# Kernel tuning notes

Measured on AMD Instinct MI355X. Metric: run time of the kernel, lower is better.

The kernel has to match this reference:

```python
import jax, jax.numpy as jnp
import numpy as np

DIM = 128
N_NODES = 50000
N_EDGES = 625000


def setup_inputs() -> dict:
    key = jax.random.key(0)
    ks = jax.random.split(key, 6)
    X = jax.random.normal(ks[0], (N_NODES, DIM), dtype=jnp.float32)
    edge_index = jax.random.randint(ks[1], (2, N_EDGES), 0, N_NODES, dtype=jnp.int64)
    # Linear params, init like torch (uniform +/- 1/sqrt(dim))
    bound = 1.0 / np.sqrt(DIM)
    msg_w = jax.random.uniform(ks[2], (DIM, DIM), minval=-bound, maxval=bound, dtype=jnp.float32)
    msg_b = jax.random.uniform(ks[3], (DIM,), minval=-bound, maxval=bound, dtype=jnp.float32)
    lin_w = jax.random.uniform(ks[4], (DIM, DIM), minval=-bound, maxval=bound, dtype=jnp.float32)
    lin_b = jax.random.uniform(ks[5], (DIM,), minval=-bound, maxval=bound, dtype=jnp.float32)
    eps = jnp.asarray(0.0, dtype=jnp.float32)
    return {"X": X, "edge_index": edge_index, "eps": eps,
            "msg_w": msg_w, "msg_b": msg_b, "lin_w": lin_w, "lin_b": lin_b}


def reference(X, edge_index, eps, msg_w, msg_b, lin_w, lin_b):
    src, dst = edge_index[0], edge_index[1]
    # msg_lin(X) then gather at dst: (E, F)
    msg = (jnp.einsum('nf,gf->ng', X, msg_w) + msg_b)[dst]
    # scatter-add messages onto src nodes: (N, F)
    agg = jax.ops.segment_sum(msg, src, num_segments=X.shape[0])
    out = (1.0 + eps) * X + agg
    out = jnp.einsum('nf,gf->ng', out, lin_w) + lin_b
    return jax.nn.relu(out)
```

## Files before the change

kernel.cpp:

```cpp
#include <hip/hip_runtime.h>
#include <hip/hip_bf16.h>

#define NN 50000
#define NE 625000
#define DIM 128

#define NBKT 782
#define NBKTP 784
#define CAP 1024
#define CHUNK 4096
#define NCHUNK ((NE + CHUNK - 1) / CHUNK)

#define XCAST_NB 6250
#define PREP_NB 65
#define SETUP_NB (NCHUNK + XCAST_NB + PREP_NB)

using fragAB = __attribute__((ext_vector_type(8))) short;
using fragC  = __attribute__((ext_vector_type(4))) float;

__device__ __forceinline__ unsigned short f2bf(float f) {
    unsigned int u = __float_as_uint(f);
    unsigned int r = u + 0x7FFFu + ((u >> 16) & 1u);
    return (unsigned short)(r >> 16);
}

__device__ __forceinline__ float bflo(unsigned v) { return __uint_as_float(v << 16); }
__device__ __forceinline__ float bfhi(unsigned v) { return __uint_as_float(v & 0xffff0000u); }

__global__ __launch_bounds__(256) void mega_setup(
    const float* __restrict__ X, const int* __restrict__ ei,
    const float* __restrict__ L, const float* __restrict__ W,
    const float* __restrict__ mb, const float* __restrict__ epsp,
    float* __restrict__ cb, unsigned short* __restrict__ Bh,
    unsigned short* __restrict__ Xbf,
    int* __restrict__ bucket_cursor, unsigned* __restrict__ staging) {
    __shared__ int cnt[NBKTP];
    __shared__ int base[NBKTP];
    __shared__ int gb[NBKTP];
    __shared__ int wsum[4];
    __shared__ unsigned staged[CHUNK];
    int blk = blockIdx.x;
    int t = threadIdx.x;

    if (blk >= NCHUNK) {
        int xb = blk - NCHUNK;
        if (xb < XCAST_NB) {
            int idx = (xb * 256 + t) * 4;
            float4 v = *(const float4*)(X + idx);
            uint2 p;
            p.x = (unsigned)f2bf(v.x) | ((unsigned)f2bf(v.y) << 16);
            p.y = (unsigned)f2bf(v.z) | ((unsigned)f2bf(v.w) << 16);
            *(uint2*)(Xbf + idx) = p;
        } else {
            int idx = (xb - XCAST_NB) * 256 + t;
            float scale = 1.0f + *epsp;
            if (idx < DIM * DIM) {
                int o = idx >> 7, g = idx & 127;
                float s = 0.f;
                for (int f = 0; f < DIM; f++) s += L[o * DIM + f] * W[f * DIM + g];
                Bh[o * 256 + 128 + g] = f2bf(s);
                Bh[o * 256 + g] = f2bf(L[o * DIM + g] * scale);
            } else if (idx < DIM * DIM + DIM) {
                int o = idx - DIM * DIM;
                float s = 0.f;
                for (int f = 0; f < DIM; f++) s += L[o * DIM + f] * mb[f];
                cb[o] = s;
            }
        }
        return;
    }

    int e0 = blk * CHUNK;
    int nthis = NE - e0; if (nthis > CHUNK) nthis = CHUNK;

    for (int i = t; i < NBKTP; i += 256) cnt[i] = 0;
    __syncthreads();

    unsigned pk[CHUNK / 256];
#pragma unroll
    for (int i = 0; i < CHUNK / 256; i++) {
        int e = e0 + i * 256 + t;
        if (e < NE) {
            int s = ei[e];
            int d = ei[NE + e];
            unsigned b = (unsigned)s >> 6;
            pk[i] = (b << 22) | ((unsigned)(s & 63) << 16) | (unsigned)d;
            atomicAdd(&cnt[b], 1);
        } else pk[i] = 0xFFFFFFFFu;
    }
    __syncthreads();

    int myb = t * 4;
    int s0 = 0;
    if (myb < NBKTP) s0 = cnt[myb] + cnt[myb + 1] + cnt[myb + 2] + cnt[myb + 3];
    int lane = t & 63, w = t >> 6;
    int v = s0;
#pragma unroll
    for (int off = 1; off < 64; off <<= 1) {
        int u = __shfl_up(v, off);
        if (lane >= off) v += u;
    }
    if (lane == 63) wsum[w] = v;
    __syncthreads();
    int add = 0;
#pragma unroll
    for (int i = 0; i < 4; i++)
        if (i < w) add += wsum[i];
    int run = v + add - s0;
    if (myb < NBKTP) {
        for (int i = 0; i < 4; i++) {
            int b = myb + i;
            base[b] = run;
            int c = cnt[b];
            gb[b] = (b < NBKT && c > 0) ? atomicAdd(&bucket_cursor[b], c) : 0;
            run += c;
        }
    }
    __syncthreads();
    if (myb < NBKTP) {
        for (int i = 0; i < 4; i++) cnt[myb + i] = base[myb + i];
    }
    __syncthreads();

#pragma unroll
    for (int i = 0; i < CHUNK / 256; i++) {
        if (pk[i] != 0xFFFFFFFFu) {
            unsigned b = pk[i] >> 22;
            int pos = atomicAdd(&cnt[b], 1);
            staged[pos] = pk[i];
        }
    }
    __syncthreads();

    for (int idx = t; idx < nthis; idx += 256) {
        unsigned p = staged[idx];
        unsigned b = p >> 22;
        int pos = gb[b] + (idx - base[b]);
        if (pos >= 0 && pos < CAP) staging[(size_t)b * CAP + pos] = p;
    }
}

__global__ __launch_bounds__(512, 8) void gather_gemm(
    const int* __restrict__ bucket_cursor, const unsigned* __restrict__ staging,
    const unsigned short* __restrict__ Xbf, const unsigned short* __restrict__ Bh,
    const float* __restrict__ cb, const float* __restrict__ lin_b,
    float* __restrict__ out) {
    __shared__ unsigned sorted_[CAP];
    __shared__ int hcnt[64];
    __shared__ int hbase[64];
    __shared__ int cur[64];
    __shared__ unsigned short As[64 * 264];
    int t = threadIdx.x;
    int b = blockIdx.x;
    int cnt_b = bucket_cursor[b];
    if (cnt_b > CAP) cnt_b = CAP;

    int xrow0 = t >> 4, xc0 = t & 15;
    int xrow1 = xrow0 + 32;
    int xnode0 = b * 64 + xrow0; if (xnode0 >= NN) xnode0 = NN - 1;
    int xnode1 = b * 64 + xrow1; if (xnode1 >= NN) xnode1 = NN - 1;
    uint4 xv0 = *(const uint4*)(Xbf + (size_t)xnode0 * 128 + xc0 * 8);
    uint4 xv1 = *(const uint4*)(Xbf + (size_t)xnode1 * 128 + xc0 * 8);

    unsigned r0 = 0xFFFFFFFFu, r1 = 0xFFFFFFFFu;
    if (t < cnt_b) r0 = staging[(size_t)b * CAP + t];
    if (t + 512 < cnt_b) r1 = staging[(size_t)b * CAP + t + 512];

    if (t < 64) hcnt[t] = 0;
    __syncthreads();
    if (r0 != 0xFFFFFFFFu) atomicAdd(&hcnt[(r0 >> 16) & 63], 1);
    if (r1 != 0xFFFFFFFFu) atomicAdd(&hcnt[(r1 >> 16) & 63], 1);
    __syncthreads();
    if (t < 64) {
        int c = hcnt[t];
        int v = c;
#pragma unroll
        for (int off = 1; off < 64; off <<= 1) {
            int u = __shfl_up(v, off);
            if (t >= off) v += u;
        }
        int ex = v - c;
        hbase[t] = ex;
        cur[t] = ex;
    }
    __syncthreads();
    if (r0 != 0xFFFFFFFFu) {
        int pos = atomicAdd(&cur[(r0 >> 16) & 63], 1);
        sorted_[pos] = r0;
    }
    if (r1 != 0xFFFFFFFFu) {
        int pos = atomicAdd(&cur[(r1 >> 16) & 63], 1);
        sorted_[pos] = r1;
    }
    *(uint4*)(As + xrow0 * 264 + xc0 * 8) = xv0;
    *(uint4*)(As + xrow1 * 264 + xc0 * 8) = xv1;
    __syncthreads();

    int wave = t >> 6, lane = t & 63;
    int q = lane >> 4, l16 = lane & 15;
    const uint4* __restrict__ X4 = (const uint4*)Xbf;
    for (int ni = 0; ni < 8; ni++) {
        int local = wave * 8 + ni;
        int node = b * 64 + local;
        if (node >= NN) continue;
        int start = hbase[local];
        int cnt = hcnt[local];
        float a0 = 0.f, a1 = 0.f, a2 = 0.f, a3 = 0.f;
        float a4 = 0.f, a5 = 0.f, a6 = 0.f, a7 = 0.f;
        int j = q;
        for (; j + 4 < cnt; j += 8) {
            int d0 = (int)(sorted_[start + j] & 0xFFFFu);
            int d1 = (int)(sorted_[start + j + 4] & 0xFFFFu);
            uint4 v0 = X4[(size_t)d0 * 16 + l16];
            uint4 v1 = X4[(size_t)d1 * 16 + l16];
            a0 += bflo(v0.x); a1 += bfhi(v0.x);
            a2 += bflo(v0.y); a3 += bfhi(v0.y);
            a4 += bflo(v0.z); a5 += bfhi(v0.z);
            a6 += bflo(v0.w); a7 += bfhi(v0.w);
            a0 += bflo(v1.x); a1 += bfhi(v1.x);
            a2 += bflo(v1.y); a3 += bfhi(v1.y);
            a4 += bflo(v1.z); a5 += bfhi(v1.z);
            a6 += bflo(v1.w); a7 += bfhi(v1.w);
        }
        if (j < cnt) {
            int d0 = (int)(sorted_[start + j] & 0xFFFFu);
            uint4 v0 = X4[(size_t)d0 * 16 + l16];
            a0 += bflo(v0.x); a1 += bfhi(v0.x);
            a2 += bflo(v0.y); a3 += bfhi(v0.y);
            a4 += bflo(v0.z); a5 += bfhi(v0.z);
            a6 += bflo(v0.w); a7 += bfhi(v0.w);
        }
        a0 += __shfl_xor(a0, 16); a1 += __shfl_xor(a1, 16);
        a2 += __shfl_xor(a2, 16); a3 += __shfl_xor(a3, 16);
        a4 += __shfl_xor(a4, 16); a5 += __shfl_xor(a5, 16);
        a6 += __shfl_xor(a6, 16); a7 += __shfl_xor(a7, 16);
        a0 += __shfl_xor(a0, 32); a1 += __shfl_xor(a1, 32);
        a2 += __shfl_xor(a2, 32); a3 += __shfl_xor(a3, 32);
        a4 += __shfl_xor(a4, 32); a5 += __shfl_xor(a5, 32);
        a6 += __shfl_xor(a6, 32); a7 += __shfl_xor(a7, 32);
        if (q == 0) {
            uint4 p;
            p.x = (unsigned)f2bf(a0) | ((unsigned)f2bf(a1) << 16);
            p.y = (unsigned)f2bf(a2) | ((unsigned)f2bf(a3) << 16);
            p.z = (unsigned)f2bf(a4) | ((unsigned)f2bf(a5) << 16);
            p.w = (unsigned)f2bf(a6) | ((unsigned)f2bf(a7) << 16);
            *(uint4*)(As + local * 264 + 128 + l16 * 8) = p;
        }
    }
    __syncthreads();

    int m16 = lane & 15;
    int quad = lane >> 4;
    int waveM = (wave & 3) * 16;
    int waveN = (wave >> 2) * 64;

    fragC acc[4];
#pragma unroll
    for (int j = 0; j < 4; j++) acc[j] = (fragC){0.f, 0.f, 0.f, 0.f};

#pragma unroll
    for (int kc = 0; kc < 8; kc++) {
        fragAB a = *(const fragAB*)(As + (waveM + m16) * 264 + kc * 32 + quad * 8);
#pragma unroll
        for (int j = 0; j < 4; j++) {
            fragAB bf = *(const fragAB*)(Bh + (size_t)(waveN + j * 16 + m16) * 256 + kc * 32 + quad * 8);
            acc[j] = __builtin_amdgcn_mfma_f32_16x16x32_bf16(a, bf, acc[j], 0, 0, 0);
        }
    }

#pragma unroll
    for (int j = 0; j < 4; j++) {
        int col = waveN + j * 16 + m16;
        float cbc = cb[col];
        float lbc = lin_b[col];
        int lr = waveM + quad * 4;
#pragma unroll
        for (int r = 0; r < 4; r++) {
            int row = lr + r;
            int node = b * 64 + row;
            if (node < NN) {
                float dg = (float)hcnt[row];
                float v = acc[j][r] + dg * cbc + lbc;
                out[(size_t)node * 128 + col] = fmaxf(v, 0.f);
            }
        }
    }
}

extern "C" void kernel_launch(void* const* d_in, const int* in_sizes, int n_in,
                              void* d_out, int out_size, void* d_ws, size_t ws_size,
                              hipStream_t stream) {
    const float* X = (const float*)d_in[0];
    const int* ei = (const int*)d_in[1];
    const float* epsp = (const float*)d_in[2];
    const float* msg_w = (const float*)d_in[3];
    const float* msg_b = (const float*)d_in[4];
    const float* lin_w = (const float*)d_in[5];
    const float* lin_b = (const float*)d_in[6];
    float* out = (float*)d_out;

    int* bucket_cursor = (int*)d_ws;
    unsigned* staging = (unsigned*)(bucket_cursor + 800);
    float* cb = (float*)(staging + (size_t)NBKT * CAP);
    unsigned short* Bh = (unsigned short*)(cb + DIM);
    unsigned short* Xbf = Bh + 128 * 256;

    hipMemsetAsync(bucket_cursor, 0, NBKTP * sizeof(int), stream);

    mega_setup<<<SETUP_NB, 256, 0, stream>>>(X, ei, lin_w, msg_w, msg_b, epsp, cb, Bh, Xbf,
                                             bucket_cursor, staging);
    gather_gemm<<<NBKT, 512, 0, stream>>>(bucket_cursor, staging, Xbf, Bh, cb, lin_b, out);
}
```

Measured before the change: 159.0 us.

## Halve bucket size to 32 nodes, unroll gather by 4, read X directly

Buckets now hold 32 source nodes instead of 64, giving about twice as many gather_gemm blocks of 256 threads each. The goal is better occupancy and load balance across CUs, with a smaller shared-memory footprint per block. The edge gather loop now issues four independent neighbor loads per iteration, padding out-of-range slots with a zero row at index NN that is cleared by an extra memset. The X half of the GEMM A-operand is read straight from global memory instead of being staged in LDS. In exchange, the setup scan covers twice as many buckets, and per-bucket capacity drops to 640, which narrows the margin against overflow.

```diff
diff --git a/kernel.cpp b/kernel.cpp
--- a/kernel.cpp
+++ b/kernel.cpp
@@ -5,9 +5,9 @@
 #define NE 625000
 #define DIM 128
 
-#define NBKT 782
-#define NBKTP 784
-#define CAP 1024
+#define NBKT 1563
+#define NBKTP 1568
+#define CAP 640
 #define CHUNK 4096
 #define NCHUNK ((NE + CHUNK - 1) / CHUNK)
 
@@ -83,16 +83,19 @@
         if (e < NE) {
             int s = ei[e];
             int d = ei[NE + e];
-            unsigned b = (unsigned)s >> 6;
-            pk[i] = (b << 22) | ((unsigned)(s & 63) << 16) | (unsigned)d;
+            unsigned b = (unsigned)s >> 5;
+            pk[i] = (b << 21) | ((unsigned)(s & 31) << 16) | (unsigned)d;
             atomicAdd(&cnt[b], 1);
         } else pk[i] = 0xFFFFFFFFu;
     }
     __syncthreads();
 
-    int myb = t * 4;
+    int myb = t * 8;
     int s0 = 0;
-    if (myb < NBKTP) s0 = cnt[myb] + cnt[myb + 1] + cnt[myb + 2] + cnt[myb + 3];
+    if (myb < NBKTP) {
+#pragma unroll
+        for (int i = 0; i < 8; i++) s0 += cnt[myb + i];
+    }
     int lane = t & 63, w = t >> 6;
     int v = s0;
 #pragma unroll
@@ -108,7 +111,7 @@
         if (i < w) add += wsum[i];
     int run = v + add - s0;
     if (myb < NBKTP) {
-        for (int i = 0; i < 4; i++) {
+        for (int i = 0; i < 8; i++) {
             int b = myb + i;
             base[b] = run;
             int c = cnt[b];
@@ -118,14 +121,14 @@
     }
     __syncthreads();
     if (myb < NBKTP) {
-        for (int i = 0; i < 4; i++) cnt[myb + i] = base[myb + i];
+        for (int i = 0; i < 8; i++) cnt[myb + i] = base[myb + i];
     }
     __syncthreads();
 
 #pragma unroll
     for (int i = 0; i < CHUNK / 256; i++) {
         if (pk[i] != 0xFFFFFFFFu) {
-            unsigned b = pk[i] >> 22;
+            unsigned b = pk[i] >> 21;
             int pos = atomicAdd(&cnt[b], 1);
             staged[pos] = pk[i];
         }
@@ -134,48 +137,43 @@
 
     for (int idx = t; idx < nthis; idx += 256) {
         unsigned p = staged[idx];
-        unsigned b = p >> 22;
+        unsigned b = p >> 21;
         int pos = gb[b] + (idx - base[b]);
         if (pos >= 0 && pos < CAP) staging[(size_t)b * CAP + pos] = p;
     }
 }
 
-__global__ __launch_bounds__(512, 8) void gather_gemm(
+__global__ __launch_bounds__(256, 8) void gather_gemm(
     const int* __restrict__ bucket_cursor, const unsigned* __restrict__ staging,
     const unsigned short* __restrict__ Xbf, const unsigned short* __restrict__ Bh,
     const float* __restrict__ cb, const float* __restrict__ lin_b,
     float* __restrict__ out) {
     __shared__ unsigned sorted_[CAP];
-    __shared__ int hcnt[64];
-    __shared__ int hbase[64];
-    __shared__ int cur[64];
-    __shared__ unsigned short As[64 * 264];
+    __shared__ int hcnt[32];
+    __shared__ int hbase[32];
+    __shared__ int cur[32];
+    __shared__ unsigned short As[32 * 136];
     int t = threadIdx.x;
     int b = blockIdx.x;
     int cnt_b = bucket_cursor[b];
     if (cnt_b > CAP) cnt_b = CAP;
 
-    int xrow0 = t >> 4, xc0 = t & 15;
-    int xrow1 = xrow0 + 32;
-    int xnode0 = b * 64 + xrow0; if (xnode0 >= NN) xnode0 = NN - 1;
-    int xnode1 = b * 64 + xrow1; if (xnode1 >= NN) xnode1 = NN - 1;
-    uint4 xv0 = *(const uint4*)(Xbf + (size_t)xnode0 * 128 + xc0 * 8);
-    uint4 xv1 = *(const uint4*)(Xbf + (size_t)xnode1 * 128 + xc0 * 8);
-
-    unsigned r0 = 0xFFFFFFFFu, r1 = 0xFFFFFFFFu;
+    unsigned r0 = 0xFFFFFFFFu, r1 = 0xFFFFFFFFu, r2 = 0xFFFFFFFFu;
     if (t < cnt_b) r0 = staging[(size_t)b * CAP + t];
-    if (t + 512 < cnt_b) r1 = staging[(size_t)b * CAP + t + 512];
-
-    if (t < 64) hcnt[t] = 0;
-    __syncthreads();
-    if (r0 != 0xFFFFFFFFu) atomicAdd(&hcnt[(r0 >> 16) & 63], 1);
-    if (r1 != 0xFFFFFFFFu) atomicAdd(&hcnt[(r1 >> 16) & 63], 1);
-    __syncthreads();
-    if (t < 64) {
+    if (t + 256 < cnt_b) r1 = staging[(size_t)b * CAP + t + 256];
+    if (t + 512 < cnt_b) r2 = staging[(size_t)b * CAP + t + 512];
+
+    if (t < 32) hcnt[t] = 0;
+    __syncthreads();
+    if (r0 != 0xFFFFFFFFu) atomicAdd(&hcnt[(r0 >> 16) & 31], 1);
+    if (r1 != 0xFFFFFFFFu) atomicAdd(&hcnt[(r1 >> 16) & 31], 1);
+    if (r2 != 0xFFFFFFFFu) atomicAdd(&hcnt[(r2 >> 16) & 31], 1);
+    __syncthreads();
+    if (t < 32) {
         int c = hcnt[t];
         int v = c;
 #pragma unroll
-        for (int off = 1; off < 64; off <<= 1) {
+        for (int off = 1; off < 32; off <<= 1) {
             int u = __shfl_up(v, off);
             if (t >= off) v += u;
         }
@@ -185,15 +183,17 @@
     }
     __syncthreads();
     if (r0 != 0xFFFFFFFFu) {
-        int pos = atomicAdd(&cur[(r0 >> 16) & 63], 1);
+        int pos = atomicAdd(&cur[(r0 >> 16) & 31], 1);
         sorted_[pos] = r0;
     }
     if (r1 != 0xFFFFFFFFu) {
-        int pos = atomicAdd(&cur[(r1 >> 16) & 63], 1);
+        int pos = atomicAdd(&cur[(r1 >> 16) & 31], 1);
         sorted_[pos] = r1;
     }
-    *(uint4*)(As + xrow0 * 264 + xc0 * 8) = xv0;
-    *(uint4*)(As + xrow1 * 264 + xc0 * 8) = xv1;
+    if (r2 != 0xFFFFFFFFu) {
+        int pos = atomicAdd(&cur[(r2 >> 16) & 31], 1);
+        sorted_[pos] = r2;
+    }
     __syncthreads();
 
     int wave = t >> 6, lane = t & 63;
@@ -201,34 +201,34 @@
     const uint4* __restrict__ X4 = (const uint4*)Xbf;
     for (int ni = 0; ni < 8; ni++) {
         int local = wave * 8 + ni;
-        int node = b * 64 + local;
+        int node = b * 32 + local;
         if (node >= NN) continue;
         int start = hbase[local];
         int cnt = hcnt[local];
         float a0 = 0.f, a1 = 0.f, a2 = 0.f, a3 = 0.f;
         float a4 = 0.f, a5 = 0.f, a6 = 0.f, a7 = 0.f;
-        int j = q;
-        for (; j + 4 < cnt; j += 8) {
-            int d0 = (int)(sorted_[start + j] & 0xFFFFu);
-            int d1 = (int)(sorted_[start + j + 4] & 0xFFFFu);
+        for (int jx = q; jx < cnt; jx += 16) {
+            int j1 = jx + 4, j2 = jx + 8, j3 = jx + 12;
+            unsigned s0v = sorted_[start + jx];
+            unsigned s1v = sorted_[start + (j1 < cnt ? j1 : 0)];
+            unsigned s2v = sorted_[start + (j2 < cnt ? j2 : 0)];
+            unsigned s3v = sorted_[start + (j3 < cnt ? j3 : 0)];
+            int d0 = (int)(s0v & 0xFFFFu);
+            int d1 = (j1 < cnt) ? (int)(s1v & 0xFFFFu) : NN;
+            int d2 = (j2 < cnt) ? (int)(s2v & 0xFFFFu) : NN;
+            int d3 = (j3 < cnt) ? (int)(s3v & 0xFFFFu) : NN;
             uint4 v0 = X4[(size_t)d0 * 16 + l16];
             uint4 v1 = X4[(size_t)d1 * 16 + l16];
-            a0 += bflo(v0.x); a1 += bfhi(v0.x);
-            a2 += bflo(v0.y); a3 += bfhi(v0.y);
-            a4 += bflo(v0.z); a5 += bfhi(v0.z);
-            a6 += bflo(v0.w); a7 += bfhi(v0.w);
-            a0 += bflo(v1.x); a1 += bfhi(v1.x);
-            a2 += bflo(v1.y); a3 += bfhi(v1.y);
-            a4 += bflo(v1.z); a5 += bfhi(v1.z);
-            a6 += bflo(v1.w); a7 += bfhi(v1.w);
-        }
-        if (j < cnt) {
-            int d0 = (int)(sorted_[start + j] & 0xFFFFu);
-            uint4 v0 = X4[(size_t)d0 * 16 + l16];
-            a0 += bflo(v0.x); a1 += bfhi(v0.x);
-            a2 += bflo(v0.y); a3 += bfhi(v0.y);
-            a4 += bflo(v0.z); a5 += bfhi(v0.z);
-            a6 += bflo(v0.w); a7 += bfhi(v0.w);
+            uint4 v2 = X4[(size_t)d2 * 16 + l16];
+            uint4 v3 = X4[(size_t)d3 * 16 + l16];
+            a0 += bflo(v0.x); a1 += bfhi(v0.x); a2 += bflo(v0.y); a3 += bfhi(v0.y);
+            a4 += bflo(v0.z); a5 += bfhi(v0.z); a6 += bflo(v0.w); a7 += bfhi(v0.w);
+            a0 += bflo(v1.x); a1 += bfhi(v1.x); a2 += bflo(v1.y); a3 += bfhi(v1.y);
+            a4 += bflo(v1.z); a5 += bfhi(v1.z); a6 += bflo(v1.w); a7 += bfhi(v1.w);
+            a0 += bflo(v2.x); a1 += bfhi(v2.x); a2 += bflo(v2.y); a3 += bfhi(v2.y);
+            a4 += bflo(v2.z); a5 += bfhi(v2.z); a6 += bflo(v2.w); a7 += bfhi(v2.w);
+            a0 += bflo(v3.x); a1 += bfhi(v3.x); a2 += bflo(v3.y); a3 += bfhi(v3.y);
+            a4 += bflo(v3.z); a5 += bfhi(v3.z); a6 += bflo(v3.w); a7 += bfhi(v3.w);
         }
         a0 += __shfl_xor(a0, 16); a1 += __shfl_xor(a1, 16);
         a2 += __shfl_xor(a2, 16); a3 += __shfl_xor(a3, 16);
@@ -244,23 +244,34 @@
             p.y = (unsigned)f2bf(a2) | ((unsigned)f2bf(a3) << 16);
             p.z = (unsigned)f2bf(a4) | ((unsigned)f2bf(a5) << 16);
             p.w = (unsigned)f2bf(a6) | ((unsigned)f2bf(a7) << 16);
-            *(uint4*)(As + local * 264 + 128 + l16 * 8) = p;
+            *(uint4*)(As + local * 136 + l16 * 8) = p;
         }
     }
     __syncthreads();
 
     int m16 = lane & 15;
     int quad = lane >> 4;
-    int waveM = (wave & 3) * 16;
-    int waveN = (wave >> 2) * 64;
+    int waveM = (wave & 1) * 16;
+    int waveN = (wave >> 1) * 64;
 
     fragC acc[4];
 #pragma unroll
     for (int j = 0; j < 4; j++) acc[j] = (fragC){0.f, 0.f, 0.f, 0.f};
 
-#pragma unroll
-    for (int kc = 0; kc < 8; kc++) {
-        fragAB a = *(const fragAB*)(As + (waveM + m16) * 264 + kc * 32 + quad * 8);
+    int xr = b * 32 + waveM + m16;
+    if (xr >= NN) xr = NN;
+#pragma unroll
+    for (int kc = 0; kc < 4; kc++) {
+        fragAB a = *(const fragAB*)(Xbf + (size_t)xr * 128 + kc * 32 + quad * 8);
+#pragma unroll
+        for (int j = 0; j < 4; j++) {
+            fragAB bf = *(const fragAB*)(Bh + (size_t)(waveN + j * 16 + m16) * 256 + kc * 32 + quad * 8);
+            acc[j] = __builtin_amdgcn_mfma_f32_16x16x32_bf16(a, bf, acc[j], 0, 0, 0);
+        }
+    }
+#pragma unroll
+    for (int kc = 4; kc < 8; kc++) {
+        fragAB a = *(const fragAB*)(As + (waveM + m16) * 136 + (kc - 4) * 32 + quad * 8);
 #pragma unroll
         for (int j = 0; j < 4; j++) {
             fragAB bf = *(const fragAB*)(Bh + (size_t)(waveN + j * 16 + m16) * 256 + kc * 32 + quad * 8);
@@ -277,7 +288,7 @@
 #pragma unroll
         for (int r = 0; r < 4; r++) {
             int row = lr + r;
-            int node = b * 64 + row;
+            int node = b * 32 + row;
             if (node < NN) {
                 float dg = (float)hcnt[row];
                 float v = acc[j][r] + dg * cbc + lbc;
@@ -300,14 +311,15 @@
     float* out = (float*)d_out;
 
     int* bucket_cursor = (int*)d_ws;
-    unsigned* staging = (unsigned*)(bucket_cursor + 800);
+    unsigned* staging = (unsigned*)(bucket_cursor + NBKTP);
     float* cb = (float*)(staging + (size_t)NBKT * CAP);
     unsigned short* Bh = (unsigned short*)(cb + DIM);
     unsigned short* Xbf = Bh + 128 * 256;
 
     hipMemsetAsync(bucket_cursor, 0, NBKTP * sizeof(int), stream);
+    hipMemsetAsync(Xbf + (size_t)NN * 128, 0, 128 * sizeof(unsigned short), stream);
 
     mega_setup<<<SETUP_NB, 256, 0, stream>>>(X, ei, lin_w, msg_w, msg_b, epsp, cb, Bh, Xbf,
                                              bucket_cursor, staging);
-    gather_gemm<<<NBKT, 512, 0, stream>>>(bucket_cursor, staging, Xbf, Bh, cb, lin_b, out);
+    gather_gemm<<<NBKT, 256, 0, stream>>>(bucket_cursor, staging, Xbf, Bh, cb, lin_b, out);
 }
```

Result: slower. 168.6 us (+6.1%).
